# Performance work log

Hardware: AMD Instinct MI355X
Metric: run time of the kernel (lower is better)

## Reference

```python
import jax, jax.numpy as jnp
import numpy as np

B, H, S, E = 1024, 64, 1, 512


def setup_inputs() -> dict:
    key = jax.random.key(0)
    k1, k2, k3, k4, k5 = jax.random.split(key, 5)
    return {
        "others1": jax.random.normal(k1, (B, H, S, E), dtype=jnp.float32),
        "others2": jax.random.normal(k2, (B, H, S, E), dtype=jnp.float32),
        "others3": jax.random.normal(k3, (B, H, S, E), dtype=jnp.float32),
        "main": jax.random.normal(k4, (B, H, S, E), dtype=jnp.float32),
        "W": jax.random.normal(k5, (E, E), dtype=jnp.float32) * 0.02,
    }


def reference(others1, others2, others3, main, W):
    # mean over the 'other' modalities, then drop the seq dim (squeeze(2))
    mean = (others1 + others2 + others3) / 3.0  # (B,H,1,E)
    m = mean[:, :, 0, :]   # (B,H,E)
    q = main[:, :, 0, :]   # (B,H,E)
    # score = mean @ W @ main^T  -> (B,H,H)
    score = jnp.einsum('bhe,ef,bgf->bhg', m, W, q)
    attn = jax.nn.softmax(score, axis=-1)          # (B,H,H)
    context = jnp.einsum('bhg,bge->bhe', attn, q)  # (B,H,E)
    return context, attn
```

## Files before the change

### kernel.cpp

```cpp
#include <hip/hip_runtime.h>
#include <hip/hip_bf16.h>

typedef _Float16 half4_t __attribute__((ext_vector_type(4)));
typedef _Float16 half8_t __attribute__((ext_vector_type(8)));
typedef float    float4_t __attribute__((ext_vector_type(4)));

#define MFMA32(a, b, c) __builtin_amdgcn_mfma_f32_16x16x32_f16((a), (b), (c), 0, 0, 0)

constexpr int  Bb  = 1024;
constexpr long CTX = (long)Bb * 64 * 512;
constexpr int  SQP = 520;
constexpr int  SMP = 520;
constexpr int  SP  = 65;
constexpr int  QTP = 72;

__global__ void w_pack(const float* __restrict__ W, _Float16* __restrict__ W2) {
    const int t = blockIdx.x * 256 + threadIdx.x;
    const int lane = t & 63, grp = t >> 6;
    const int E = grp >> 4, c = grp & 15;
    const int r16 = lane & 15, q = lane >> 4;
    const float* src = W + (long)(E * 16 + r16) * 512 + c * 32 + q * 8;
    float4_t x = *(const float4_t*)(src);
    float4_t y = *(const float4_t*)(src + 4);
    half8_t h;
    h[0]=(_Float16)x[0]; h[1]=(_Float16)x[1]; h[2]=(_Float16)x[2]; h[3]=(_Float16)x[3];
    h[4]=(_Float16)y[0]; h[5]=(_Float16)y[1]; h[6]=(_Float16)y[2]; h[7]=(_Float16)y[3];
    *(half8_t*)(W2 + (long)t * 8) = h;
}

__global__ __launch_bounds__(512, 2)
void ovo_score(const float* __restrict__ o1, const float* __restrict__ o2,
               const float* __restrict__ o3, const float* __restrict__ qm,
               const _Float16* __restrict__ W2, float* __restrict__ out)
{
    __shared__ __align__(16) _Float16 sQ[64 * SQP];
    __shared__ __align__(16) _Float16 sM[2][16 * SMP];

    const int t = threadIdx.x, lane = t & 63, w = t >> 6;
    const int r16 = lane & 15, q = lane >> 4;
    const int gt = w & 3, eh = w >> 2;
    const long base = (long)blockIdx.x * 64 * 512;
    const float4_t zf4 = {0.f, 0.f, 0.f, 0.f};

    float4_t rA[12], rB[12];
    #define OLOAD(R, hc) do { \
        const long fb = base + (long)(hc) * 8192 + (long)t * 4; \
        _Pragma("unroll") for (int i = 0; i < 4; ++i) R[i]     = *(const float4_t*)(o1 + fb + i * 2048); \
        _Pragma("unroll") for (int i = 0; i < 4; ++i) R[4 + i] = *(const float4_t*)(o2 + fb + i * 2048); \
        _Pragma("unroll") for (int i = 0; i < 4; ++i) R[8 + i] = *(const float4_t*)(o3 + fb + i * 2048); \
    } while (0)
    #define OCOMMIT(R, buf) do { \
        _Pragma("unroll") for (int i = 0; i < 4; ++i) { \
            float4_t m = (R[i] + R[4 + i] + R[8 + i]) * (1.0f / 3.0f); \
            half4_t h; \
            h[0]=(_Float16)m[0]; h[1]=(_Float16)m[1]; h[2]=(_Float16)m[2]; h[3]=(_Float16)m[3]; \
            *(half4_t*)(&sM[buf][(i * 4 + (t >> 7)) * SMP + (t & 127) * 4]) = h; \
        } \
    } while (0)

    {
        const long qb = base + (long)t * 4;
        #pragma unroll
        for (int k = 0; k < 16; ++k) {
            float4_t v = *(const float4_t*)(qm + qb + (long)k * 2048);
            half4_t h;
            h[0]=(_Float16)v[0]; h[1]=(_Float16)v[1]; h[2]=(_Float16)v[2]; h[3]=(_Float16)v[3];
            *(half4_t*)(&sQ[(k * 4 + (t >> 7)) * SQP + (t & 127) * 4]) = h;
        }
    }
    OLOAD(rA, 0);
    __syncthreads();

    float4_t vacc[4][4];
    #pragma unroll
    for (int i = 0; i < 4; ++i)
        #pragma unroll
        for (int j = 0; j < 4; ++j) vacc[i][j] = zf4;

    #pragma unroll
    for (int c = 0; c < 16; ++c) {
        half8_t Aq[4], Bw[4];
        #pragma unroll
        for (int g2 = 0; g2 < 4; ++g2)
            Aq[g2] = *(const half8_t*)(&sQ[(g2 * 16 + r16) * SQP + c * 32 + q * 8]);
        #pragma unroll
        for (int et = 0; et < 4; ++et)
            Bw[et] = *(const half8_t*)(W2 + (long)((w * 4 + et) * 16 + c) * 512 + lane * 8);
        #pragma unroll
        for (int g2 = 0; g2 < 4; ++g2)
            #pragma unroll
            for (int et = 0; et < 4; ++et)
                vacc[g2][et] = MFMA32(Aq[g2], Bw[et], vacc[g2][et]);
    }
    __syncthreads();

    #pragma unroll
    for (int g2 = 0; g2 < 4; ++g2)
        #pragma unroll
        for (int et = 0; et < 4; ++et)
            #pragma unroll
            for (int r = 0; r < 4; ++r)
                sQ[(g2 * 16 + q * 4 + r) * SQP + w * 64 + et * 16 + r16] =
                    (_Float16)vacc[g2][et][r];
    OCOMMIT(rA, 0);
    OLOAD(rB, 1);
    __syncthreads();

    float4_t acc0 = zf4, acc1 = zf4, acc2 = zf4, acc3 = zf4;
    #define SCHUNK(ACC, buf) do { \
        _Pragma("unroll") for (int c = 0; c < 8; ++c) { \
            const int cc = eh * 8 + c; \
            half8_t af = *(const half8_t*)(&sM[buf][r16 * SMP + cc * 32 + q * 8]); \
            half8_t bf = *(const half8_t*)(&sQ[(gt * 16 + r16) * SQP + cc * 32 + q * 8]); \
            ACC = MFMA32(af, bf, ACC); \
        } \
    } while (0)

    SCHUNK(acc0, 0); OCOMMIT(rB, 1); OLOAD(rA, 2);
    __syncthreads();
    SCHUNK(acc1, 1); OCOMMIT(rA, 0); OLOAD(rB, 3);
    __syncthreads();
    SCHUNK(acc2, 0); OCOMMIT(rB, 1);
    __syncthreads();
    SCHUNK(acc3, 1);
    __syncthreads();

    float4_t* part4 = reinterpret_cast<float4_t*>(&sM[0][0]);
    float*    sS    = reinterpret_cast<float*>(&sQ[0]);
    if (eh == 1) {
        part4[(gt * 4 + 0) * 64 + lane] = acc0;
        part4[(gt * 4 + 1) * 64 + lane] = acc1;
        part4[(gt * 4 + 2) * 64 + lane] = acc2;
        part4[(gt * 4 + 3) * 64 + lane] = acc3;
    }
    __syncthreads();
    if (eh == 0) {
        acc0 += part4[(gt * 4 + 0) * 64 + lane];
        acc1 += part4[(gt * 4 + 1) * 64 + lane];
        acc2 += part4[(gt * 4 + 2) * 64 + lane];
        acc3 += part4[(gt * 4 + 3) * 64 + lane];
        #pragma unroll
        for (int r = 0; r < 4; ++r) {
            sS[( 0 + q * 4 + r) * SP + gt * 16 + r16] = acc0[r];
            sS[(16 + q * 4 + r) * SP + gt * 16 + r16] = acc1[r];
            sS[(32 + q * 4 + r) * SP + gt * 16 + r16] = acc2[r];
            sS[(48 + q * 4 + r) * SP + gt * 16 + r16] = acc3[r];
        }
    }
    __syncthreads();

    if (w < 4) {
        const int r  = w * 16 + r16;
        const int qd = lane >> 4;
        const float* srow = sS + r * SP + qd * 16;
        float v[16];
        float mx = -1e30f;
        #pragma unroll
        for (int i = 0; i < 16; ++i) { v[i] = srow[i]; mx = fmaxf(mx, v[i]); }
        mx = fmaxf(mx, __shfl_xor(mx, 16));
        mx = fmaxf(mx, __shfl_xor(mx, 32));
        float sum = 0.f;
        #pragma unroll
        for (int i = 0; i < 16; ++i) { v[i] = __expf(v[i] - mx); sum += v[i]; }
        sum += __shfl_xor(sum, 16);
        sum += __shfl_xor(sum, 32);
        const float inv = 1.0f / sum;
        float* aout = out + CTX + ((long)blockIdx.x * 64 + r) * 64 + qd * 16;
        #pragma unroll
        for (int i = 0; i < 16; ++i) aout[i] = v[i] * inv;
    }
}

__global__ __launch_bounds__(256, 4)
void ovo_ctx(const float* __restrict__ qm, const float* __restrict__ out_attn,
             float* __restrict__ out)
{
    __shared__ __align__(16) _Float16 qT[2][64 * QTP];

    const int t = threadIdx.x, lane = t & 63, w = t >> 6;
    const int r16 = lane & 15, q = lane >> 4;
    const long b = blockIdx.x;
    const long base = b * 64 * 512;
    const float4_t zf4 = {0.f, 0.f, 0.f, 0.f};

    const float* ap = out_attn + (b * 64 + w * 16 + r16) * 64 + q * 8;
    half8_t pA0, pA1;
    {
        float4_t x = *(const float4_t*)(ap + 0),  y = *(const float4_t*)(ap + 4);
        pA0[0]=(_Float16)x[0]; pA0[1]=(_Float16)x[1]; pA0[2]=(_Float16)x[2]; pA0[3]=(_Float16)x[3];
        pA0[4]=(_Float16)y[0]; pA0[5]=(_Float16)y[1]; pA0[6]=(_Float16)y[2]; pA0[7]=(_Float16)y[3];
        float4_t z = *(const float4_t*)(ap + 32), u = *(const float4_t*)(ap + 36);
        pA1[0]=(_Float16)z[0]; pA1[1]=(_Float16)z[1]; pA1[2]=(_Float16)z[2]; pA1[3]=(_Float16)z[3];
        pA1[4]=(_Float16)u[0]; pA1[5]=(_Float16)u[1]; pA1[6]=(_Float16)u[2]; pA1[7]=(_Float16)u[3];
    }

    const int sg = t & 63, se = (t >> 6) * 16;
    const float* qsrc = qm + base + (long)sg * 512 + se;
    float4_t rA[4], rB[4];

    #define QLOAD(R, c) do { \
        _Pragma("unroll") \
        for (int i = 0; i < 4; ++i) R[i] = *(const float4_t*)(qsrc + (c) * 64 + i * 4); \
    } while (0)
    #define QCOMMIT(R, buf) do { \
        _Pragma("unroll") \
        for (int i = 0; i < 4; ++i) \
            _Pragma("unroll") \
            for (int jj = 0; jj < 4; ++jj) \
                qT[buf][(se + i * 4 + jj) * QTP + sg] = (_Float16)R[i][jj]; \
    } while (0)
    #define BCOMP(c, buf) do { \
        _Pragma("unroll") \
        for (int et = 0; et < 4; ++et) { \
            half8_t b0 = *(const half8_t*)(&qT[buf][(et * 16 + r16) * QTP + q * 8]); \
            half8_t b1 = *(const half8_t*)(&qT[buf][(et * 16 + r16) * QTP + 32 + q * 8]); \
            float4_t acc = MFMA32(pA0, b0, zf4); \
            acc = MFMA32(pA1, b1, acc); \
            _Pragma("unroll") \
            for (int rr = 0; rr < 4; ++rr) \
                out[(b * 64 + w * 16 + q * 4 + rr) * 512 + (c) * 64 + et * 16 + r16] = acc[rr]; \
        } \
    } while (0)

    QLOAD(rA, 0);
    QCOMMIT(rA, 0);
    __syncthreads();
    #pragma unroll
    for (int cc = 0; cc < 8; cc += 2) {
        QLOAD(rB, cc + 1);
        BCOMP(cc, 0);
        QCOMMIT(rB, 1);
        __syncthreads();
        if (cc + 2 < 8) QLOAD(rA, cc + 2);
        BCOMP(cc + 1, 1);
        if (cc + 2 < 8) QCOMMIT(rA, 0);
        __syncthreads();
    }
}

extern "C" void kernel_launch(void* const* d_in, const int* in_sizes, int n_in,
                              void* d_out, int out_size, void* d_ws, size_t ws_size,
                              hipStream_t stream) {
    const float* o1 = (const float*)d_in[0];
    const float* o2 = (const float*)d_in[1];
    const float* o3 = (const float*)d_in[2];
    const float* qm = (const float*)d_in[3];
    const float* W  = (const float*)d_in[4];
    float* out = (float*)d_out;
    _Float16* W2 = (_Float16*)d_ws;

    w_pack<<<dim3(128), dim3(256), 0, stream>>>(W, W2);
    ovo_score<<<dim3(Bb), dim3(512), 0, stream>>>(o1, o2, o3, qm, W2, out);
    ovo_ctx<<<dim3(Bb), dim3(256), 0, stream>>>(qm, out + CTX, out);
}
```

Before: 198.7 us.

## Split score kernel into V-projection kernel and finer-grained score/softmax kernel

```diff
diff --git a/kernel.cpp b/kernel.cpp
--- a/kernel.cpp
+++ b/kernel.cpp
@@ -10,9 +10,8 @@
 constexpr int  Bb  = 1024;
 constexpr long CTX = (long)Bb * 64 * 512;
 constexpr int  SQP = 520;
-constexpr int  SMP = 520;
-constexpr int  SP  = 65;
 constexpr int  QTP = 72;
+constexpr long V2OFF = 524288;
 
 __global__ void w_pack(const float* __restrict__ W, _Float16* __restrict__ W2) {
     const int t = blockIdx.x * 256 + threadIdx.x;
@@ -28,35 +27,16 @@
     *(half8_t*)(W2 + (long)t * 8) = h;
 }
 
-__global__ __launch_bounds__(512, 2)
-void ovo_score(const float* __restrict__ o1, const float* __restrict__ o2,
-               const float* __restrict__ o3, const float* __restrict__ qm,
-               const _Float16* __restrict__ W2, float* __restrict__ out)
+__global__ __launch_bounds__(512, 3)
+void ovo_v(const float* __restrict__ qm, const _Float16* __restrict__ W2,
+           _Float16* __restrict__ V2)
 {
     __shared__ __align__(16) _Float16 sQ[64 * SQP];
-    __shared__ __align__(16) _Float16 sM[2][16 * SMP];
 
     const int t = threadIdx.x, lane = t & 63, w = t >> 6;
     const int r16 = lane & 15, q = lane >> 4;
-    const int gt = w & 3, eh = w >> 2;
     const long base = (long)blockIdx.x * 64 * 512;
     const float4_t zf4 = {0.f, 0.f, 0.f, 0.f};
-
-    float4_t rA[12], rB[12];
-    #define OLOAD(R, hc) do { \
-        const long fb = base + (long)(hc) * 8192 + (long)t * 4; \
-        _Pragma("unroll") for (int i = 0; i < 4; ++i) R[i]     = *(const float4_t*)(o1 + fb + i * 2048); \
-        _Pragma("unroll") for (int i = 0; i < 4; ++i) R[4 + i] = *(const float4_t*)(o2 + fb + i * 2048); \
-        _Pragma("unroll") for (int i = 0; i < 4; ++i) R[8 + i] = *(const float4_t*)(o3 + fb + i * 2048); \
-    } while (0)
-    #define OCOMMIT(R, buf) do { \
-        _Pragma("unroll") for (int i = 0; i < 4; ++i) { \
-            float4_t m = (R[i] + R[4 + i] + R[8 + i]) * (1.0f / 3.0f); \
-            half4_t h; \
-            h[0]=(_Float16)m[0]; h[1]=(_Float16)m[1]; h[2]=(_Float16)m[2]; h[3]=(_Float16)m[3]; \
-            *(half4_t*)(&sM[buf][(i * 4 + (t >> 7)) * SMP + (t & 127) * 4]) = h; \
-        } \
-    } while (0)
 
     {
         const long qb = base + (long)t * 4;
@@ -68,7 +48,6 @@
             *(half4_t*)(&sQ[(k * 4 + (t >> 7)) * SQP + (t & 127) * 4]) = h;
         }
     }
-    OLOAD(rA, 0);
     __syncthreads();
 
     float4_t vacc[4][4];
@@ -102,57 +81,92 @@
             for (int r = 0; r < 4; ++r)
                 sQ[(g2 * 16 + q * 4 + r) * SQP + w * 64 + et * 16 + r16] =
                     (_Float16)vacc[g2][et][r];
-    OCOMMIT(rA, 0);
-    OLOAD(rB, 1);
-    __syncthreads();
+    __syncthreads();
+
+    _Float16* vdst = V2 + (long)blockIdx.x * 32768;
+    #pragma unroll
+    for (int i = 0; i < 8; ++i) {
+        const int grp = w * 8 + i;
+        const int gt = grp >> 4, cc = grp & 15;
+        half8_t hv = *(const half8_t*)(&sQ[(gt * 16 + r16) * SQP + cc * 32 + q * 8]);
+        *(half8_t*)(vdst + (long)grp * 512 + lane * 8) = hv;
+    }
+}
+
+__global__ __launch_bounds__(256, 4)
+void ovo_s(const float* __restrict__ o1, const float* __restrict__ o2,
+           const float* __restrict__ o3, const _Float16* __restrict__ V2,
+           float* __restrict__ out)
+{
+    __shared__ float sRed[4][16 * 68];
+
+    const int t = threadIdx.x, lane = t & 63, w = t >> 6;
+    const int r16 = lane & 15, q = lane >> 4;
+    const int b  = blockIdx.x >> 2;
+    const int hq = blockIdx.x & 3;
+    const long base = (long)b * 64 * 512;
+    const long abase = base + (long)(hq * 16 + r16) * 512 + w * 128 + q * 8;
+    const _Float16* vb = V2 + (long)b * 32768;
+    const float4_t zf4 = {0.f, 0.f, 0.f, 0.f};
 
     float4_t acc0 = zf4, acc1 = zf4, acc2 = zf4, acc3 = zf4;
-    #define SCHUNK(ACC, buf) do { \
-        _Pragma("unroll") for (int c = 0; c < 8; ++c) { \
-            const int cc = eh * 8 + c; \
-            half8_t af = *(const half8_t*)(&sM[buf][r16 * SMP + cc * 32 + q * 8]); \
-            half8_t bf = *(const half8_t*)(&sQ[(gt * 16 + r16) * SQP + cc * 32 + q * 8]); \
-            ACC = MFMA32(af, bf, ACC); \
-        } \
-    } while (0)
-
-    SCHUNK(acc0, 0); OCOMMIT(rB, 1); OLOAD(rA, 2);
-    __syncthreads();
-    SCHUNK(acc1, 1); OCOMMIT(rA, 0); OLOAD(rB, 3);
-    __syncthreads();
-    SCHUNK(acc2, 0); OCOMMIT(rB, 1);
-    __syncthreads();
-    SCHUNK(acc3, 1);
-    __syncthreads();
-
-    float4_t* part4 = reinterpret_cast<float4_t*>(&sM[0][0]);
-    float*    sS    = reinterpret_cast<float*>(&sQ[0]);
-    if (eh == 1) {
-        part4[(gt * 4 + 0) * 64 + lane] = acc0;
-        part4[(gt * 4 + 1) * 64 + lane] = acc1;
-        part4[(gt * 4 + 2) * 64 + lane] = acc2;
-        part4[(gt * 4 + 3) * 64 + lane] = acc3;
-    }
-    __syncthreads();
-    if (eh == 0) {
-        acc0 += part4[(gt * 4 + 0) * 64 + lane];
-        acc1 += part4[(gt * 4 + 1) * 64 + lane];
-        acc2 += part4[(gt * 4 + 2) * 64 + lane];
-        acc3 += part4[(gt * 4 + 3) * 64 + lane];
-        #pragma unroll
-        for (int r = 0; r < 4; ++r) {
-            sS[( 0 + q * 4 + r) * SP + gt * 16 + r16] = acc0[r];
-            sS[(16 + q * 4 + r) * SP + gt * 16 + r16] = acc1[r];
-            sS[(32 + q * 4 + r) * SP + gt * 16 + r16] = acc2[r];
-            sS[(48 + q * 4 + r) * SP + gt * 16 + r16] = acc3[r];
-        }
-    }
-    __syncthreads();
-
-    if (w < 4) {
-        const int r  = w * 16 + r16;
-        const int qd = lane >> 4;
-        const float* srow = sS + r * SP + qd * 16;
+    float4_t a1A, b1A, a2A, b2A, a3A, b3A;
+    float4_t a1B, b1B, a2B, b2B, a3B, b3B;
+
+    #define SLOAD(S, c) do { \
+        const long o_ = abase + (c) * 32; \
+        a1##S = *(const float4_t*)(o1 + o_); b1##S = *(const float4_t*)(o1 + o_ + 4); \
+        a2##S = *(const float4_t*)(o2 + o_); b2##S = *(const float4_t*)(o2 + o_ + 4); \
+        a3##S = *(const float4_t*)(o3 + o_); b3##S = *(const float4_t*)(o3 + o_ + 4); \
+    } while (0)
+
+    #define SCOMP(S, c) do { \
+        float4_t m0 = (a1##S + a2##S + a3##S) * (1.0f / 3.0f); \
+        float4_t m1 = (b1##S + b2##S + b3##S) * (1.0f / 3.0f); \
+        half8_t af; \
+        af[0]=(_Float16)m0[0]; af[1]=(_Float16)m0[1]; af[2]=(_Float16)m0[2]; af[3]=(_Float16)m0[3]; \
+        af[4]=(_Float16)m1[0]; af[5]=(_Float16)m1[1]; af[6]=(_Float16)m1[2]; af[7]=(_Float16)m1[3]; \
+        half8_t bf0 = *(const half8_t*)(vb + (long)(0 * 16 + w * 4 + (c)) * 512 + lane * 8); \
+        half8_t bf1 = *(const half8_t*)(vb + (long)(1 * 16 + w * 4 + (c)) * 512 + lane * 8); \
+        half8_t bf2 = *(const half8_t*)(vb + (long)(2 * 16 + w * 4 + (c)) * 512 + lane * 8); \
+        half8_t bf3 = *(const half8_t*)(vb + (long)(3 * 16 + w * 4 + (c)) * 512 + lane * 8); \
+        acc0 = MFMA32(af, bf0, acc0); \
+        acc1 = MFMA32(af, bf1, acc1); \
+        acc2 = MFMA32(af, bf2, acc2); \
+        acc3 = MFMA32(af, bf3, acc3); \
+    } while (0)
+
+    SLOAD(A, 0); SLOAD(B, 1);
+    SCOMP(A, 0); SLOAD(A, 2);
+    SCOMP(B, 1); SLOAD(B, 3);
+    SCOMP(A, 2);
+    SCOMP(B, 3);
+
+    #pragma unroll
+    for (int r = 0; r < 4; ++r) {
+        sRed[w][(q * 4 + r) * 68 +  0 + r16] = acc0[r];
+        sRed[w][(q * 4 + r) * 68 + 16 + r16] = acc1[r];
+        sRed[w][(q * 4 + r) * 68 + 32 + r16] = acc2[r];
+        sRed[w][(q * 4 + r) * 68 + 48 + r16] = acc3[r];
+    }
+    __syncthreads();
+    if (w == 0) {
+        for (int i = 0; i < 17; ++i)
+            sRed[0][lane + i * 64] += sRed[2][lane + i * 64];
+    }
+    if (w == 1) {
+        for (int i = 0; i < 17; ++i)
+            sRed[1][lane + i * 64] += sRed[3][lane + i * 64];
+    }
+    __syncthreads();
+    if (w == 0) {
+        for (int i = 0; i < 17; ++i)
+            sRed[0][lane + i * 64] += sRed[1][lane + i * 64];
+    }
+    __syncthreads();
+
+    if (w == 0) {
+        const float* srow = &sRed[0][r16 * 68 + q * 16];
         float v[16];
         float mx = -1e30f;
         #pragma unroll
@@ -165,7 +179,7 @@
         sum += __shfl_xor(sum, 16);
         sum += __shfl_xor(sum, 32);
         const float inv = 1.0f / sum;
-        float* aout = out + CTX + ((long)blockIdx.x * 64 + r) * 64 + qd * 16;
+        float* aout = out + CTX + ((long)b * 64 + hq * 16 + r16) * 64 + q * 16;
         #pragma unroll
         for (int i = 0; i < 16; ++i) aout[i] = v[i] * inv;
     }
@@ -248,8 +262,10 @@
     const float* W  = (const float*)d_in[4];
     float* out = (float*)d_out;
     _Float16* W2 = (_Float16*)d_ws;
+    _Float16* V2 = (_Float16*)d_ws + V2OFF;
 
     w_pack<<<dim3(128), dim3(256), 0, stream>>>(W, W2);
-    ovo_score<<<dim3(Bb), dim3(512), 0, stream>>>(o1, o2, o3, qm, W2, out);
+    ovo_v<<<dim3(Bb), dim3(512), 0, stream>>>(qm, W2, V2);
+    ovo_s<<<dim3(Bb * 4), dim3(256), 0, stream>>>(o1, o2, o3, V2, out);
     ovo_ctx<<<dim3(Bb), dim3(256), 0, stream>>>(qm, out + CTX, out);
 }
```

New measurement: 258.5 us. +30.1%, slower.
